# Kernel tuning notes

Hardware: AMD Instinct MI355X
Metric: run time of the kernel (lower is better)

Reference implementation:

```python
import jax, jax.numpy as jnp
import numpy as np
from jax import lax

B, CIN, COUT, H, W = 4, 32, 64, 192, 192
K = 3  # kernel size
RED = 16  # SE reduction
EPS = 1e-5


def _conv2d_same(x, w, b):
    y = lax.conv_general_dilated(x, w, (1, 1), 'SAME',
                                 dimension_numbers=('NCHW', 'OIHW', 'NCHW'))
    return y + b[None, :, None, None]


def _bilinear_gather(x, py, px):
    # x: [B,C,H,W]; py/px: [B,KK,H,W] absolute sample coords -> [B,C,KK,H,W]
    Bb, C, Hh, Ww = x.shape
    KK = py.shape[1]
    y0 = jnp.floor(py); x0 = jnp.floor(px)
    wy = py - y0; wx = px - x0
    x_flat = x.reshape(Bb, C, Hh * Ww)

    def corner(yi, xi, wgt):
        valid = (yi >= 0) & (yi < Hh) & (xi >= 0) & (xi < Ww)
        yc = jnp.clip(yi, 0, Hh - 1).astype(jnp.int32)
        xc = jnp.clip(xi, 0, Ww - 1).astype(jnp.int32)
        idx = (yc * Ww + xc).reshape(Bb, 1, KK * Hh * Ww)
        g = jnp.take_along_axis(x_flat, idx, axis=2).reshape(Bb, C, KK, Hh, Ww)
        w_eff = (wgt * valid.astype(x.dtype))[:, None]  # [B,1,KK,H,W]
        return g * w_eff

    out = (corner(y0, x0, (1 - wy) * (1 - wx))
           + corner(y0, x0 + 1, (1 - wy) * wx)
           + corner(y0 + 1, x0, wy * (1 - wx))
           + corner(y0 + 1, x0 + 1, wy * wx))
    return out  # [B,C,KK,H,W]


def _deform_conv(x, offsets, w, b):
    # torchvision DeformConv2d, stride 1, pad 1, dilation 1, 1 offset group.
    Bb, C, Hh, Ww = x.shape
    off = offsets.reshape(Bb, K * K, 2, Hh, Ww)
    dy, dx = off[:, :, 0], off[:, :, 1]  # [B,KK,H,W]
    ky, kx = jnp.meshgrid(jnp.arange(K) - 1, jnp.arange(K) - 1, indexing='ij')
    hg, wg = jnp.meshgrid(jnp.arange(Hh), jnp.arange(Ww), indexing='ij')
    py = hg[None, None] + ky.reshape(-1)[None, :, None, None] + dy
    px = wg[None, None] + kx.reshape(-1)[None, :, None, None] + dx
    sampled = _bilinear_gather(x, py, px)  # [B,CIN,KK,H,W]
    y = jnp.einsum('bckhw,ock->bohw', sampled, w.reshape(w.shape[0], C, K * K))
    return y + b[None, :, None, None]


def _forward(x, w_off, b_off, w_def, b_def, bn_gamma, bn_beta,
             fc1_w, fc1_b, fc2_w, fc2_b):
    offsets = _conv2d_same(x, w_off, b_off)
    y = _deform_conv(x, offsets, w_def, b_def)
    # BatchNorm2d (training-mode batch statistics)
    mean = jnp.mean(y, axis=(0, 2, 3), keepdims=True)
    var = jnp.var(y, axis=(0, 2, 3), keepdims=True)
    y = (y - mean) * lax.rsqrt(var + EPS)
    y = y * bn_gamma[None, :, None, None] + bn_beta[None, :, None, None]
    # SE layer
    s = jnp.mean(y, axis=(2, 3))  # [B,C]
    s = jax.nn.relu(s @ fc1_w.T + fc1_b)
    s = jax.nn.sigmoid(s @ fc2_w.T + fc2_b)
    y = y * s[:, :, None, None]
    y = jax.nn.relu(y)
    # MaxPool 2x2 stride 2
    y = lax.reduce_window(y, -jnp.inf, lax.max, (1, 1, 2, 2), (1, 1, 2, 2), 'VALID')
    return y


def setup_inputs() -> dict:
    key = jax.random.key(0)
    ks = jax.random.split(key, 12)
    rn = lambda k, s, sc=1.0: (jax.random.normal(k, s, dtype=jnp.float32) * sc)
    return {
        'x': rn(ks[0], (B, CIN, H, W)),
        'w_off': rn(ks[1], (2 * K * K, CIN, K, K), 0.02),
        'b_off': jnp.zeros((2 * K * K,), jnp.float32),
        'w_def': rn(ks[2], (COUT, CIN, K, K), 0.05),
        'b_def': rn(ks[3], (COUT,), 0.05),
        'bn_gamma': jnp.ones((COUT,), jnp.float32),
        'bn_beta': jnp.zeros((COUT,), jnp.float32),
        'fc1_w': rn(ks[4], (COUT // RED, COUT), 0.1),
        'fc1_b': jnp.zeros((COUT // RED,), jnp.float32),
        'fc2_w': rn(ks[5], (COUT, COUT // RED), 0.1),
        'fc2_b': jnp.zeros((COUT,), jnp.float32),
    }


def reference(x, w_off, b_off, w_def, b_def, bn_gamma, bn_beta,
              fc1_w, fc1_b, fc2_w, fc2_b):
    return _forward(x, w_off, b_off, w_def, b_def, bn_gamma, bn_beta,
                    fc1_w, fc1_b, fc2_w, fc2_b)
```

## Files before the change

kernel.cpp:

```cpp
#include <hip/hip_runtime.h>
#include <math.h>

#define B_    4
#define CIN_  32
#define COUT_ 64
#define H_    192
#define W_    192
#define HW_   (H_ * W_)
#define NPIX_ (B_ * HW_)
#define EPS_  1e-5f

typedef _Float16 half8 __attribute__((ext_vector_type(8)));
typedef float    f32x4 __attribute__((ext_vector_type(4)));

#define WTN_ 18432
#define NSTAT_ 4096

static __device__ __forceinline__ int swz2304(int blk) {
    return ((blk & 7) * 288) + (blk >> 3);
}

__global__ __launch_bounds__(256) void k_pre(
    const float* __restrict__ x, const float* __restrict__ w_def,
    const float* __restrict__ w_off, float* __restrict__ xt,
    _Float16* __restrict__ wt_def, float* __restrict__ wt_off,
    float* __restrict__ stats)
{
    if (blockIdx.x < NPIX_ / 256) {
        __shared__ float lds[32 * 257];
        const int tid  = threadIdx.x;
        const int pid0 = blockIdx.x * 256;
        const int b    = pid0 / HW_;
        const int rem0 = pid0 - b * HW_;
        const float* xb = x + (size_t)b * CIN_ * HW_ + rem0;

#pragma unroll
        for (int c = 0; c < 32; ++c)
            lds[c * 257 + tid] = xb[c * HW_ + tid];
        __syncthreads();

        float4* dst = (float4*)(xt + (size_t)pid0 * 32);
#pragma unroll
        for (int i = 0; i < 8; ++i) {
            const int idx = i * 256 + tid;
            const int px  = idx >> 3;
            const int q   = idx & 7;
            float4 v;
            v.x = lds[(q * 4 + 0) * 257 + px];
            v.y = lds[(q * 4 + 1) * 257 + px];
            v.z = lds[(q * 4 + 2) * 257 + px];
            v.w = lds[(q * 4 + 3) * 257 + px];
            dst[idx] = v;
        }
    } else {
        const int i = (blockIdx.x - NPIX_ / 256) * 256 + threadIdx.x;
        if (i < WTN_) {
            const int j  = i & 7;
            const int ln = (i >> 3) & 63;
            const int ot = (i >> 9) & 3;
            const int kk = i >> 11;
            const int o  = ot * 16 + (ln & 15);
            const int c  = (ln >> 4) * 8 + j;
            const float wv = w_def[(o * 32 + c) * 9 + kk];
            const _Float16 hi = (_Float16)wv;
            wt_def[i]        = hi;
            wt_def[WTN_ + i] = (_Float16)(wv - (float)hi);
        } else if (i < WTN_ + 5760) {
            const int e  = i - WTN_;
            const int c  = e & 31;
            const int t  = e >> 5;
            const int o  = t % 20;
            const int kk = t / 20;
            wt_off[e] = (o < 18) ? w_off[(o * 32 + c) * 9 + kk] : 0.f;
        } else if (i < WTN_ + 5760 + NSTAT_) {
            stats[i - WTN_ - 5760] = 0.f;
        }
    }
}

__global__ __launch_bounds__(256, 6) void k_fused(
    const float* __restrict__ xt, const float* __restrict__ wto,
    const float* __restrict__ b_off, const _Float16* __restrict__ wtd,
    const float* __restrict__ b_def, float* __restrict__ y,
    float* __restrict__ sum_bc, float* __restrict__ sumsq_bc)
{
    __shared__ __align__(16) float smem[3168];
    float4 (*tile)[198] = (float4(*)[198])smem;
    float* offlds = smem;
    float* red_s  = smem + 2048;
    float* red_q  = smem + 2304;

    const int tid  = threadIdx.x;
    const int px   = tid & 63;
    const int og   = __builtin_amdgcn_readfirstlane(tid >> 6);
    const int lane = tid & 63;

    const int blk  = swz2304(blockIdx.x);
    const int base = blk * 64;
    const int b    = base / HW_;
    const int rem0 = base - b * HW_;
    const int h0   = rem0 / W_;
    const int w0   = rem0 - h0 * W_;
    const float* xb = xt + (size_t)b * HW_ * 32;

    float acc5[5] = {0.f, 0.f, 0.f, 0.f, 0.f};
    const bool rv0 = (h0 - 1 >= 0), rv2 = (h0 + 1 < H_);

#pragma unroll 1
    for (int hf = 0; hf < 2; ++hf) {
        for (int i = tid; i < 792; i += 256) {
            const int j   = i & 3;
            const int rec = i >> 2;
            const int r   = rec / 66;
            const int cc  = rec - r * 66;
            const int hc  = min(max(h0 + r - 1, 0), H_ - 1);
            const int wc  = min(max(w0 + cc - 1, 0), W_ - 1);
            tile[j][rec] = *(const float4*)(xb + (hc * W_ + wc) * 32 + hf * 16 + j * 4);
        }
        __syncthreads();

#pragma unroll 1
        for (int kk = 0; kk < 9; ++kk) {
            const int ky = kk / 3, kx = kk % 3;
            const bool rok = (ky == 0) ? rv0 : ((ky == 2) ? rv2 : true);
            const int wcol = w0 + px + kx - 1;
            const float g = (rok && wcol >= 0 && wcol < W_) ? 1.f : 0.f;
            const int rec = ky * 66 + px + kx;

            float4 v[4];
#pragma unroll
            for (int j = 0; j < 4; ++j) {
                v[j] = tile[j][rec];
                v[j].x *= g; v[j].y *= g; v[j].z *= g; v[j].w *= g;
            }
            const float* wk = wto + (kk * 20 + og * 5) * 32 + hf * 16;
#pragma unroll
            for (int oo = 0; oo < 5; ++oo) {
                const float4* wr = (const float4*)(wk + oo * 32);
                float s = acc5[oo];
#pragma unroll
                for (int j = 0; j < 4; ++j) {
                    const float4 wv = wr[j];
                    s += v[j].x * wv.x + v[j].y * wv.y
                       + v[j].z * wv.z + v[j].w * wv.w;
                }
                acc5[oo] = s;
            }
        }
        __syncthreads();
    }

#pragma unroll
    for (int oo = 0; oo < 5; ++oo) {
        const int o = og * 5 + oo;
        if (o < 18) offlds[o * 64 + px] = acc5[oo] + b_off[o];
    }
    __syncthreads();

    const int l15 = lane & 15;
    const int lq4 = lane >> 4;
    const int pxl = (og << 4) + l15;
    const int wc_ = w0 + pxl;
    const float* xg = xb + lq4 * 8;
    const _Float16* wbh = wtd + lane * 8;
    const _Float16* wbl = wtd + WTN_ + lane * 8;

    f32x4 acc[4];
#pragma unroll
    for (int ot = 0; ot < 4; ++ot) acc[ot] = (f32x4){0.f, 0.f, 0.f, 0.f};

#pragma unroll 1
    for (int kk = 0; kk < 9; ++kk) {
        const _Float16* wkh = wbh + (kk << 11);
        const _Float16* wkl = wbl + (kk << 11);
        const half8 bh0 = *(const half8*)(wkh);
        const half8 bh1 = *(const half8*)(wkh + 512);
        const half8 bh2 = *(const half8*)(wkh + 1024);
        const half8 bh3 = *(const half8*)(wkh + 1536);
        const half8 bl0 = *(const half8*)(wkl);
        const half8 bl1 = *(const half8*)(wkl + 512);
        const half8 bl2 = *(const half8*)(wkl + 1024);
        const half8 bl3 = *(const half8*)(wkl + 1536);

        const float dy = offlds[(2 * kk) * 64 + pxl];
        const float dx = offlds[(2 * kk + 1) * 64 + pxl];
        const float py = (float)(h0 + kk / 3 - 1) + dy;
        const float qx = (float)(wc_ + kk % 3 - 1) + dx;
        const float y0f = floorf(py), x0f = floorf(qx);
        const float wy = py - y0f, wx = qx - x0f;
        const int iy0 = (int)y0f, ix0 = (int)x0f;
        const int iy1 = iy0 + 1,  ix1 = ix0 + 1;
        const float vy0 = (iy0 >= 0 && iy0 < H_) ? 1.f : 0.f;
        const float vy1 = (iy1 >= 0 && iy1 < H_) ? 1.f : 0.f;
        const float vx0 = (ix0 >= 0 && ix0 < W_) ? 1.f : 0.f;
        const float vx1 = (ix1 >= 0 && ix1 < W_) ? 1.f : 0.f;
        const float w00 = (1.f - wy) * (1.f - wx) * vy0 * vx0;
        const float w01 = (1.f - wy) * wx * vy0 * vx1;
        const float w10 = wy * (1.f - wx) * vy1 * vx0;
        const float w11 = wy * wx * vy1 * vx1;
        const int cy0 = min(max(iy0, 0), H_ - 1), cy1 = min(max(iy1, 0), H_ - 1);
        const int cx0 = min(max(ix0, 0), W_ - 1), cx1 = min(max(ix1, 0), W_ - 1);
        const int o00 = (cy0 * W_ + cx0) * 32, o01 = (cy0 * W_ + cx1) * 32;
        const int o10 = (cy1 * W_ + cx0) * 32, o11 = (cy1 * W_ + cx1) * 32;

        const float4 A0 = *(const float4*)(xg + o00), A1 = *(const float4*)(xg + o00 + 4);
        const float4 B0 = *(const float4*)(xg + o01), B1 = *(const float4*)(xg + o01 + 4);
        const float4 C0 = *(const float4*)(xg + o10), C1 = *(const float4*)(xg + o10 + 4);
        const float4 D0 = *(const float4*)(xg + o11), D1 = *(const float4*)(xg + o11 + 4);

        float v[8];
        v[0] = w00 * A0.x + w01 * B0.x + w10 * C0.x + w11 * D0.x;
        v[1] = w00 * A0.y + w01 * B0.y + w10 * C0.y + w11 * D0.y;
        v[2] = w00 * A0.z + w01 * B0.z + w10 * C0.z + w11 * D0.z;
        v[3] = w00 * A0.w + w01 * B0.w + w10 * C0.w + w11 * D0.w;
        v[4] = w00 * A1.x + w01 * B1.x + w10 * C1.x + w11 * D1.x;
        v[5] = w00 * A1.y + w01 * B1.y + w10 * C1.y + w11 * D1.y;
        v[6] = w00 * A1.z + w01 * B1.z + w10 * C1.z + w11 * D1.z;
        v[7] = w00 * A1.w + w01 * B1.w + w10 * C1.w + w11 * D1.w;

        half8 a_hi, a_lo;
#pragma unroll
        for (int j = 0; j < 8; ++j) {
            const _Float16 h = (_Float16)v[j];
            a_hi[j] = h;
            a_lo[j] = (_Float16)(v[j] - (float)h);
        }

        acc[0] = __builtin_amdgcn_mfma_f32_16x16x32_f16(a_hi, bh0, acc[0], 0, 0, 0);
        acc[1] = __builtin_amdgcn_mfma_f32_16x16x32_f16(a_hi, bh1, acc[1], 0, 0, 0);
        acc[2] = __builtin_amdgcn_mfma_f32_16x16x32_f16(a_hi, bh2, acc[2], 0, 0, 0);
        acc[3] = __builtin_amdgcn_mfma_f32_16x16x32_f16(a_hi, bh3, acc[3], 0, 0, 0);
        acc[0] = __builtin_amdgcn_mfma_f32_16x16x32_f16(a_lo, bh0, acc[0], 0, 0, 0);
        acc[1] = __builtin_amdgcn_mfma_f32_16x16x32_f16(a_lo, bh1, acc[1], 0, 0, 0);
        acc[2] = __builtin_amdgcn_mfma_f32_16x16x32_f16(a_lo, bh2, acc[2], 0, 0, 0);
        acc[3] = __builtin_amdgcn_mfma_f32_16x16x32_f16(a_lo, bh3, acc[3], 0, 0, 0);
        acc[0] = __builtin_amdgcn_mfma_f32_16x16x32_f16(a_hi, bl0, acc[0], 0, 0, 0);
        acc[1] = __builtin_amdgcn_mfma_f32_16x16x32_f16(a_hi, bl1, acc[1], 0, 0, 0);
        acc[2] = __builtin_amdgcn_mfma_f32_16x16x32_f16(a_hi, bl2, acc[2], 0, 0, 0);
        acc[3] = __builtin_amdgcn_mfma_f32_16x16x32_f16(a_hi, bl3, acc[3], 0, 0, 0);
    }

    const int rem = rem0 + (og << 4) + (lq4 << 2);
    float sred[4], qred[4];
#pragma unroll
    for (int ot = 0; ot < 4; ++ot) {
        const float bias = b_def[ot * 16 + l15];
        f32x4 av = acc[ot];
        av[0] += bias; av[1] += bias; av[2] += bias; av[3] += bias;
        *(f32x4*)(y + ((size_t)(b * COUT_ + ot * 16 + l15)) * HW_ + rem) = av;
        float s = av[0] + av[1] + av[2] + av[3];
        float q = av[0] * av[0] + av[1] * av[1] + av[2] * av[2] + av[3] * av[3];
        s += __shfl_xor(s, 16, 64); s += __shfl_xor(s, 32, 64);
        q += __shfl_xor(q, 16, 64); q += __shfl_xor(q, 32, 64);
        sred[ot] = s; qred[ot] = q;
    }
    float ms = sred[0], mq = qred[0];
    if (lq4 == 1)      { ms = sred[1]; mq = qred[1]; }
    else if (lq4 == 2) { ms = sred[2]; mq = qred[2]; }
    else if (lq4 == 3) { ms = sred[3]; mq = qred[3]; }

    red_s[(og << 6) + lane] = ms;
    red_q[(og << 6) + lane] = mq;
    __syncthreads();
    if (og == 0) {
        const float s = red_s[lane] + red_s[64 + lane]
                      + red_s[128 + lane] + red_s[192 + lane];
        const float q = red_q[lane] + red_q[64 + lane]
                      + red_q[128 + lane] + red_q[192 + lane];
        const int slot = ((blockIdx.x & 7) << 8) + (b << 6) + lane;
        atomicAdd(&sum_bc[slot], s);
        atomicAdd(&sumsq_bc[slot], q);
    }
}

__global__ __launch_bounds__(256) void k_finish(
    const float* __restrict__ y,
    const float* __restrict__ sum_bc, const float* __restrict__ sumsq_bc,
    const float* __restrict__ gamma, const float* __restrict__ beta,
    const float* __restrict__ fc1_w, const float* __restrict__ fc1_b,
    const float* __restrict__ fc2_w, const float* __restrict__ fc2_b,
    float* __restrict__ out)
{
    __shared__ float sal[256], sbb[256], sin_[256], ssum[256], qsum[256];
    const int tid = threadIdx.x;
    {
        const int b = tid >> 6, c = tid & 63;
        float s_bc = 0.f, q_bc = 0.f;
#pragma unroll
        for (int p = 0; p < 8; ++p) {
            s_bc += sum_bc[(p << 8) + tid];
            q_bc += sumsq_bc[(p << 8) + tid];
        }
        ssum[tid] = s_bc; qsum[tid] = q_bc;
        __syncthreads();
        const float ch_s = ssum[c] + ssum[64 + c] + ssum[128 + c] + ssum[192 + c];
        const float ch_q = qsum[c] + qsum[64 + c] + qsum[128 + c] + qsum[192 + c];
        const float invN = 1.f / (float)(B_ * HW_);
        const float mean = ch_s * invN;
        const float var  = ch_q * invN - mean * mean;
        const float a    = gamma[c] * rsqrtf(var + EPS_);
        const float bi   = beta[c] - mean * a;
        sin_[tid] = a * (s_bc * (1.f / (float)HW_)) + bi;
        __syncthreads();
        float hv[4];
#pragma unroll
        for (int j = 0; j < 4; ++j) {
            float hs = fc1_b[j];
            for (int cc = 0; cc < 64; ++cc)
                hs += sin_[b * 64 + cc] * fc1_w[j * 64 + cc];
            hv[j] = fmaxf(hs, 0.f);
        }
        float o = fc2_b[c];
#pragma unroll
        for (int j = 0; j < 4; ++j) o += hv[j] * fc2_w[c * 4 + j];
        const float s = 1.f / (1.f + expf(-o));
        sal[tid] = a * s;
        sbb[tid] = bi * s;
    }
    __syncthreads();

    const int t    = blockIdx.x * 256 + tid;
    const int opix = t * 2;
    const int bc   = opix / (96 * 96);
    const int rem  = opix - bc * (96 * 96);
    const int oh   = rem / 96, ow = rem - oh * 96;
    const float al = sal[bc], bb = sbb[bc];
    const float* yp = y + (size_t)bc * HW_ + (2 * oh) * W_ + 2 * ow;
    const float4 r0 = *(const float4*)yp;
    const float4 r1 = *(const float4*)(yp + W_);
    float2 st;
    st.x = fmaxf(fmaxf(fmaxf(fmaf(r0.x, al, bb), fmaf(r0.y, al, bb)),
                       fmaxf(fmaf(r1.x, al, bb), fmaf(r1.y, al, bb))), 0.f);
    st.y = fmaxf(fmaxf(fmaxf(fmaf(r0.z, al, bb), fmaf(r0.w, al, bb)),
                       fmaxf(fmaf(r1.z, al, bb), fmaf(r1.w, al, bb))), 0.f);
    *(float2*)(out + opix) = st;
}

extern "C" void kernel_launch(void* const* d_in, const int* in_sizes, int n_in,
                              void* d_out, int out_size, void* d_ws, size_t ws_size,
                              hipStream_t stream)
{
    const float* x     = (const float*)d_in[0];
    const float* w_off = (const float*)d_in[1];
    const float* b_off = (const float*)d_in[2];
    const float* w_def = (const float*)d_in[3];
    const float* b_def = (const float*)d_in[4];
    const float* gamma = (const float*)d_in[5];
    const float* beta  = (const float*)d_in[6];
    const float* fc1_w = (const float*)d_in[7];
    const float* fc1_b = (const float*)d_in[8];
    const float* fc2_w = (const float*)d_in[9];
    const float* fc2_b = (const float*)d_in[10];
    float* out = (float*)d_out;

    float* ws   = (float*)d_ws;
    float* yb        = ws;
    float* xt        = yb + 9437184;
    _Float16* wt_def = (_Float16*)(xt + 4718592);
    float* wt_off    = xt + 4718592 + 18432;
    float* stats     = wt_off + 5760;
    float* sum_bc    = stats;
    float* sumsq_bc  = stats + 2048;

    k_pre   <<<dim3(NPIX_ / 256 + 111), dim3(256), 0, stream>>>(
                x, w_def, w_off, xt, wt_def, wt_off, stats);
    k_fused <<<dim3(NPIX_ / 64), dim3(256), 0, stream>>>(
                xt, wt_off, b_off, wt_def, b_def, yb, sum_bc, sumsq_bc);
    k_finish<<<dim3(B_ * COUT_ * 96 * 96 / 512), dim3(256), 0, stream>>>(
                yb, sum_bc, sumsq_bc, gamma, beta,
                fc1_w, fc1_b, fc2_w, fc2_b, out);
}
```

Before: 238.2 us.

## Split fused offset-conv and deformable-conv kernel into two kernels via workspace

Splits the fused kernel into two. The first computes the 18-channel offset convolution and writes it to a workspace buffer. The second reads those offsets and does the bilinear gather plus the split-precision MFMA deform conv with BN statistics. The intent is to cut per-kernel register and LDS pressure so the deform kernel can run at higher occupancy (launch bounds 8). The cost is an extra launch and a write and read of about 2.6M offset floats. The old fused path is kept as a fallback for when the workspace is too small.

```diff
diff --git a/kernel.cpp b/kernel.cpp
--- a/kernel.cpp
+++ b/kernel.cpp
@@ -15,6 +15,7 @@
 
 #define WTN_ 18432
 #define NSTAT_ 4096
+#define NOFF_ (18 * NPIX_)
 
 static __device__ __forceinline__ int swz2304(int blk) {
     return ((blk & 7) * 288) + (blk >> 3);
@@ -78,6 +79,213 @@
     }
 }
 
+__global__ __launch_bounds__(256, 4) void k_offsets(
+    const float* __restrict__ xt, const float* __restrict__ wto,
+    const float* __restrict__ b_off, float* __restrict__ offs)
+{
+    __shared__ __align__(16) float smem[6336];
+    float4 (*tile)[198] = (float4(*)[198])smem;
+
+    const int tid  = threadIdx.x;
+    const int px   = tid & 63;
+    const int og   = __builtin_amdgcn_readfirstlane(tid >> 6);
+
+    const int blk  = swz2304(blockIdx.x);
+    const int base = blk * 64;
+    const int b    = base / HW_;
+    const int rem0 = base - b * HW_;
+    const int h0   = rem0 / W_;
+    const int w0   = rem0 - h0 * W_;
+    const float* xb = xt + (size_t)b * HW_ * 32;
+
+    for (int i = tid; i < 1584; i += 256) {
+        const int j   = i & 7;
+        const int rec = i >> 3;
+        const int r   = rec / 66;
+        const int cc  = rec - r * 66;
+        const int hc  = min(max(h0 + r - 1, 0), H_ - 1);
+        const int wc  = min(max(w0 + cc - 1, 0), W_ - 1);
+        tile[j][rec] = *(const float4*)(xb + (hc * W_ + wc) * 32 + j * 4);
+    }
+    __syncthreads();
+
+    float acc5[5] = {0.f, 0.f, 0.f, 0.f, 0.f};
+    const bool rv0 = (h0 - 1 >= 0), rv2 = (h0 + 1 < H_);
+#pragma unroll 1
+    for (int kk = 0; kk < 9; ++kk) {
+        const int ky = kk / 3, kx = kk % 3;
+        const bool rok = (ky == 0) ? rv0 : ((ky == 2) ? rv2 : true);
+        const int wcol = w0 + px + kx - 1;
+        const float g = (rok && wcol >= 0 && wcol < W_) ? 1.f : 0.f;
+        const int rec = ky * 66 + px + kx;
+
+        float4 v[8];
+#pragma unroll
+        for (int j = 0; j < 8; ++j) {
+            v[j] = tile[j][rec];
+            v[j].x *= g; v[j].y *= g; v[j].z *= g; v[j].w *= g;
+        }
+        const float* wk = wto + (kk * 20 + og * 5) * 32;
+#pragma unroll
+        for (int oo = 0; oo < 5; ++oo) {
+            const float4* wr = (const float4*)(wk + oo * 32);
+            float s = acc5[oo];
+#pragma unroll
+            for (int j = 0; j < 8; ++j) {
+                const float4 wv = wr[j];
+                s += v[j].x * wv.x + v[j].y * wv.y
+                   + v[j].z * wv.z + v[j].w * wv.w;
+            }
+            acc5[oo] = s;
+        }
+    }
+#pragma unroll
+    for (int oo = 0; oo < 5; ++oo) {
+        const int o = og * 5 + oo;
+        if (o < 18)
+            offs[(b * 18 + o) * HW_ + rem0 + px] = acc5[oo] + b_off[o];
+    }
+}
+
+__global__ __launch_bounds__(256, 8) void k_deform(
+    const float* __restrict__ xt, const float* __restrict__ offs,
+    const _Float16* __restrict__ wtd, const float* __restrict__ b_def,
+    float* __restrict__ y, float* __restrict__ sum_bc,
+    float* __restrict__ sumsq_bc)
+{
+    __shared__ float red[512];
+    float* red_s = red;
+    float* red_q = red + 256;
+
+    const int tid  = threadIdx.x;
+    const int og   = __builtin_amdgcn_readfirstlane(tid >> 6);
+    const int lane = tid & 63;
+
+    const int blk  = swz2304(blockIdx.x);
+    const int base = blk * 64;
+    const int b    = base / HW_;
+    const int rem0 = base - b * HW_;
+    const int h0   = rem0 / W_;
+    const int w0   = rem0 - h0 * W_;
+    const float* xb = xt + (size_t)b * HW_ * 32;
+
+    const int l15 = lane & 15;
+    const int lq4 = lane >> 4;
+    const int pxl = (og << 4) + l15;
+    const int wc_ = w0 + pxl;
+    const float* xg = xb + lq4 * 8;
+    const _Float16* wbh = wtd + lane * 8;
+    const _Float16* wbl = wtd + WTN_ + lane * 8;
+    const float* offp = offs + b * 18 * HW_ + rem0 + pxl;
+
+    f32x4 acc[4];
+#pragma unroll
+    for (int ot = 0; ot < 4; ++ot) acc[ot] = (f32x4){0.f, 0.f, 0.f, 0.f};
+
+#pragma unroll 1
+    for (int kk = 0; kk < 9; ++kk) {
+        const _Float16* wkh = wbh + (kk << 11);
+        const _Float16* wkl = wbl + (kk << 11);
+        const half8 bh0 = *(const half8*)(wkh);
+        const half8 bh1 = *(const half8*)(wkh + 512);
+        const half8 bh2 = *(const half8*)(wkh + 1024);
+        const half8 bh3 = *(const half8*)(wkh + 1536);
+        const half8 bl0 = *(const half8*)(wkl);
+        const half8 bl1 = *(const half8*)(wkl + 512);
+        const half8 bl2 = *(const half8*)(wkl + 1024);
+        const half8 bl3 = *(const half8*)(wkl + 1536);
+
+        const float dy = offp[(2 * kk) * HW_];
+        const float dx = offp[(2 * kk + 1) * HW_];
+        const float py = (float)(h0 + kk / 3 - 1) + dy;
+        const float qx = (float)(wc_ + kk % 3 - 1) + dx;
+        const float y0f = floorf(py), x0f = floorf(qx);
+        const float wy = py - y0f, wx = qx - x0f;
+        const int iy0 = (int)y0f, ix0 = (int)x0f;
+        const int iy1 = iy0 + 1,  ix1 = ix0 + 1;
+        const float vy0 = (iy0 >= 0 && iy0 < H_) ? 1.f : 0.f;
+        const float vy1 = (iy1 >= 0 && iy1 < H_) ? 1.f : 0.f;
+        const float vx0 = (ix0 >= 0 && ix0 < W_) ? 1.f : 0.f;
+        const float vx1 = (ix1 >= 0 && ix1 < W_) ? 1.f : 0.f;
+        const float w00 = (1.f - wy) * (1.f - wx) * vy0 * vx0;
+        const float w01 = (1.f - wy) * wx * vy0 * vx1;
+        const float w10 = wy * (1.f - wx) * vy1 * vx0;
+        const float w11 = wy * wx * vy1 * vx1;
+        const int cy0 = min(max(iy0, 0), H_ - 1), cy1 = min(max(iy1, 0), H_ - 1);
+        const int cx0 = min(max(ix0, 0), W_ - 1), cx1 = min(max(ix1, 0), W_ - 1);
+        const int o00 = (cy0 * W_ + cx0) * 32, o01 = (cy0 * W_ + cx1) * 32;
+        const int o10 = (cy1 * W_ + cx0) * 32, o11 = (cy1 * W_ + cx1) * 32;
+
+        const float4 A0 = *(const float4*)(xg + o00), A1 = *(const float4*)(xg + o00 + 4);
+        const float4 B0 = *(const float4*)(xg + o01), B1 = *(const float4*)(xg + o01 + 4);
+        const float4 C0 = *(const float4*)(xg + o10), C1 = *(const float4*)(xg + o10 + 4);
+        const float4 D0 = *(const float4*)(xg + o11), D1 = *(const float4*)(xg + o11 + 4);
+
+        float v[8];
+        v[0] = w00 * A0.x + w01 * B0.x + w10 * C0.x + w11 * D0.x;
+        v[1] = w00 * A0.y + w01 * B0.y + w10 * C0.y + w11 * D0.y;
+        v[2] = w00 * A0.z + w01 * B0.z + w10 * C0.z + w11 * D0.z;
+        v[3] = w00 * A0.w + w01 * B0.w + w10 * C0.w + w11 * D0.w;
+        v[4] = w00 * A1.x + w01 * B1.x + w10 * C1.x + w11 * D1.x;
+        v[5] = w00 * A1.y + w01 * B1.y + w10 * C1.y + w11 * D1.y;
+        v[6] = w00 * A1.z + w01 * B1.z + w10 * C1.z + w11 * D1.z;
+        v[7] = w00 * A1.w + w01 * B1.w + w10 * C1.w + w11 * D1.w;
+
+        half8 a_hi, a_lo;
+#pragma unroll
+        for (int j = 0; j < 8; ++j) {
+            const _Float16 h = (_Float16)v[j];
+            a_hi[j] = h;
+            a_lo[j] = (_Float16)(v[j] - (float)h);
+        }
+
+        acc[0] = __builtin_amdgcn_mfma_f32_16x16x32_f16(a_hi, bh0, acc[0], 0, 0, 0);
+        acc[1] = __builtin_amdgcn_mfma_f32_16x16x32_f16(a_hi, bh1, acc[1], 0, 0, 0);
+        acc[2] = __builtin_amdgcn_mfma_f32_16x16x32_f16(a_hi, bh2, acc[2], 0, 0, 0);
+        acc[3] = __builtin_amdgcn_mfma_f32_16x16x32_f16(a_hi, bh3, acc[3], 0, 0, 0);
+        acc[0] = __builtin_amdgcn_mfma_f32_16x16x32_f16(a_lo, bh0, acc[0], 0, 0, 0);
+        acc[1] = __builtin_amdgcn_mfma_f32_16x16x32_f16(a_lo, bh1, acc[1], 0, 0, 0);
+        acc[2] = __builtin_amdgcn_mfma_f32_16x16x32_f16(a_lo, bh2, acc[2], 0, 0, 0);
+        acc[3] = __builtin_amdgcn_mfma_f32_16x16x32_f16(a_lo, bh3, acc[3], 0, 0, 0);
+        acc[0] = __builtin_amdgcn_mfma_f32_16x16x32_f16(a_hi, bl0, acc[0], 0, 0, 0);
+        acc[1] = __builtin_amdgcn_mfma_f32_16x16x32_f16(a_hi, bl1, acc[1], 0, 0, 0);
+        acc[2] = __builtin_amdgcn_mfma_f32_16x16x32_f16(a_hi, bl2, acc[2], 0, 0, 0);
+        acc[3] = __builtin_amdgcn_mfma_f32_16x16x32_f16(a_hi, bl3, acc[3], 0, 0, 0);
+    }
+
+    const int rem = rem0 + (og << 4) + (lq4 << 2);
+    float sred[4], qred[4];
+#pragma unroll
+    for (int ot = 0; ot < 4; ++ot) {
+        const float bias = b_def[ot * 16 + l15];
+        f32x4 av = acc[ot];
+        av[0] += bias; av[1] += bias; av[2] += bias; av[3] += bias;
+        *(f32x4*)(y + ((size_t)(b * COUT_ + ot * 16 + l15)) * HW_ + rem) = av;
+        float s = av[0] + av[1] + av[2] + av[3];
+        float q = av[0] * av[0] + av[1] * av[1] + av[2] * av[2] + av[3] * av[3];
+        s += __shfl_xor(s, 16, 64); s += __shfl_xor(s, 32, 64);
+        q += __shfl_xor(q, 16, 64); q += __shfl_xor(q, 32, 64);
+        sred[ot] = s; qred[ot] = q;
+    }
+    float ms = sred[0], mq = qred[0];
+    if (lq4 == 1)      { ms = sred[1]; mq = qred[1]; }
+    else if (lq4 == 2) { ms = sred[2]; mq = qred[2]; }
+    else if (lq4 == 3) { ms = sred[3]; mq = qred[3]; }
+
+    red_s[(og << 6) + lane] = ms;
+    red_q[(og << 6) + lane] = mq;
+    __syncthreads();
+    if (og == 0) {
+        const float s = red_s[lane] + red_s[64 + lane]
+                      + red_s[128 + lane] + red_s[192 + lane];
+        const float q = red_q[lane] + red_q[64 + lane]
+                      + red_q[128 + lane] + red_q[192 + lane];
+        const int slot = ((blockIdx.x & 7) << 8) + (b << 6) + lane;
+        atomicAdd(&sum_bc[slot], s);
+        atomicAdd(&sumsq_bc[slot], q);
+    }
+}
+
 __global__ __launch_bounds__(256, 6) void k_fused(
     const float* __restrict__ xt, const float* __restrict__ wto,
     const float* __restrict__ b_off, const _Float16* __restrict__ wtd,
@@ -361,11 +569,24 @@
     float* stats     = wt_off + 5760;
     float* sum_bc    = stats;
     float* sumsq_bc  = stats + 2048;
-
-    k_pre   <<<dim3(NPIX_ / 256 + 111), dim3(256), 0, stream>>>(
-                x, w_def, w_off, xt, wt_def, wt_off, stats);
-    k_fused <<<dim3(NPIX_ / 64), dim3(256), 0, stream>>>(
-                xt, wt_off, b_off, wt_def, b_def, yb, sum_bc, sumsq_bc);
+    float* offs      = stats + NSTAT_;
+
+    const size_t need = ((size_t)9437184 + 4718592 + 18432 + 5760 + NSTAT_
+                         + NOFF_) * sizeof(float);
+
+    k_pre <<<dim3(NPIX_ / 256 + 111), dim3(256), 0, stream>>>(
+              x, w_def, w_off, xt, wt_def, wt_off, stats);
+
+    if (ws_size >= need) {
+        k_offsets<<<dim3(NPIX_ / 64), dim3(256), 0, stream>>>(
+                    xt, wt_off, b_off, offs);
+        k_deform <<<dim3(NPIX_ / 64), dim3(256), 0, stream>>>(
+                    xt, offs, wt_def, b_def, yb, sum_bc, sumsq_bc);
+    } else {
+        k_fused  <<<dim3(NPIX_ / 64), dim3(256), 0, stream>>>(
+                    xt, wt_off, b_off, wt_def, b_def, yb, sum_bc, sumsq_bc);
+    }
+
     k_finish<<<dim3(B_ * COUT_ * 96 * 96 / 512), dim3(256), 0, stream>>>(
                 yb, sum_bc, sumsq_bc, gamma, beta,
                 fc1_w, fc1_b, fc2_w, fc2_b, out);
```

New measurement: 261.5 us. 1.1x slower.
